# Kernel tuning notes

Measured on AMD Instinct MI355X. Metric: run time of the kernel, lower is better.

Reference implementation:

```python
import math
import jax, jax.numpy as jnp
import numpy as np

B, I, D, H, K, MAXI, FF = 2, 1024, 1024, 16, 64, 1024, 4096
DH = D // H
EPS = 1e-5

def _ln(x, g, b):
    m = x.mean(-1, keepdims=True)
    v = ((x - m) ** 2).mean(-1, keepdims=True)
    return (x - m) / jnp.sqrt(v + EPS) * g + b

def setup_inputs() -> dict:
    key = jax.random.key(0)
    ks = jax.random.split(key, 16)
    p = lambda i, sh: (0.02 * jax.random.normal(ks[i], sh)).astype(jnp.float32)
    # clamped relative-position indices: clamp(j - floor(1.0*i), -K, K) + K
    ar = np.arange(MAXI)
    idx = np.clip(ar[None, :] - ar[:, None], -K, K) + K  # [maxI, maxI]
    return {
        'x': jax.random.normal(ks[0], (B, I, D), dtype=jnp.float32),
        'j': jax.random.normal(ks[1], (B, I, D), dtype=jnp.float32),
        'ln1_g': jnp.ones((D,), jnp.float32), 'ln1_b': jnp.zeros((D,), jnp.float32),
        'Wv_w': p(2, (D, D)), 'Wv_b': jnp.zeros((D,), jnp.float32),
        'Wg_w': p(3, (D, D)), 'Wg_b': jnp.zeros((D,), jnp.float32),
        'lnv_g': jnp.ones((D,), jnp.float32), 'lnv_b': jnp.zeros((D,), jnp.float32),
        'Wq1_w': p(4, (D, D)), 'Wq1_b': jnp.zeros((D,), jnp.float32),
        'Wk_w': p(5, (D, D)), 'Wk_b': jnp.zeros((D,), jnp.float32),
        'Wq2_w': p(6, (D, D)), 'Wq2_b': jnp.zeros((D,), jnp.float32),
        'rel_emb': p(7, (2 * K + 1, D)),
        'Wo_w': p(8, (D, D)), 'Wo_b': jnp.zeros((D,), jnp.float32),
        'ln2_g': jnp.ones((D,), jnp.float32), 'ln2_b': jnp.zeros((D,), jnp.float32),
        'ff1_w': p(9, (D, FF)), 'ff1_b': jnp.zeros((FF,), jnp.float32),
        'ff2_w': p(10, (FF, D)), 'ff2_b': jnp.zeros((D,), jnp.float32),
        'indices': jnp.asarray(idx, jnp.int32),
    }

def reference(x, j, ln1_g, ln1_b, Wv_w, Wv_b, Wg_w, Wg_b, lnv_g, lnv_b,
              Wq1_w, Wq1_b, Wk_w, Wk_b, Wq2_w, Wq2_b, rel_emb,
              Wo_w, Wo_b, ln2_g, ln2_b, ff1_w, ff1_b, ff2_w, ff2_b, indices):
    Bv, Iq, _ = x.shape
    res = x
    xn = _ln(x, ln1_g, ln1_b)
    # value / gate streams with gelu activation, layernorm on v only
    v = _ln(jax.nn.gelu(xn @ Wv_w + Wv_b, approximate=False), lnv_g, lnv_b)
    g = jax.nn.gelu(xn @ Wg_w + Wg_b, approximate=False)
    vh = v.reshape(Bv, -1, H, DH)   # [B,J,H,Dh]
    gh = g.reshape(Bv, -1, H, DH)   # [B,I,H,Dh]
    # absolute-position scores: Q1(j) . K(j)^T
    q1 = (j @ Wq1_w + Wq1_b).reshape(Bv, -1, H, DH)
    kh = (j @ Wk_w + Wk_b).reshape(Bv, -1, H, DH)
    aa = jnp.einsum('bihd,bjhd->bhij', q1, kh)  # [B,H,I,J]
    # relative-position scores: Q2(j) . rel_embed^T, gathered by clamped indices
    q2 = (j @ Wq2_w + Wq2_b).reshape(Bv, -1, H, DH)
    rh = rel_emb.reshape(2 * K + 1, H, DH)
    arf = jnp.einsum('bihd,rhd->bhir', q2, rh)  # [B,H,I,2K+1]
    Jk = kh.shape[1]
    idx = jnp.broadcast_to(indices[None, None, :Iq, :Jk], (Bv, H, Iq, Jk))
    ar = jnp.take_along_axis(arf, idx, axis=-1)  # [B,H,I,J]
    a = jax.nn.softmax((aa + ar) / math.sqrt(DH), axis=-1)
    o = jnp.einsum('bhij,bjhd->bihd', a, vh) * gh  # gated attention output
    o = o.reshape(Bv, -1, D) @ Wo_w + Wo_b
    x1 = o + res
    # feed-forward sublayer
    h = jax.nn.relu(_ln(x1, ln2_g, ln2_b) @ ff1_w + ff1_b)
    out = h @ ff2_w + ff2_b + x1
    return (out, a)
```

## Files before the change

kernel.cpp:

```cpp
#include <hip/hip_runtime.h>
#include <hip/hip_bf16.h>
#include <math.h>

#define D_   1024
#define H_   16
#define DH_  64
#define FF_  4096
#define R_   129
#define I_   1024
#define B_   2
#define MROWS 2048
#define QKVLD 3072

typedef __bf16 v8bf16 __attribute__((ext_vector_type(8)));
typedef float f32x4 __attribute__((ext_vector_type(4)));

__device__ __forceinline__ float gelu_f(float x) {
    return 0.5f * x * (1.0f + erff(x * 0.7071067811865476f));
}

__device__ __forceinline__ void ldsld16(const void* g, void* l) {
    __builtin_amdgcn_global_load_lds(
        (const __attribute__((address_space(1))) void*)g,
        (__attribute__((address_space(3))) void*)l, 16, 0, 0);
}

__global__ __launch_bounds__(256) void cvt_bf16(const float* __restrict__ in,
        __hip_bfloat16* __restrict__ out, int n4) {
    int i = blockIdx.x * 256 + threadIdx.x;
    if (i >= n4) return;
    float4 v = reinterpret_cast<const float4*>(in)[i];
    union { __hip_bfloat16 h[4]; uint2 u; } pk;
    pk.h[0] = __float2bfloat16(v.x); pk.h[1] = __float2bfloat16(v.y);
    pk.h[2] = __float2bfloat16(v.z); pk.h[3] = __float2bfloat16(v.w);
    reinterpret_cast<uint2*>(out)[i] = pk.u;
}

__global__ __launch_bounds__(256) void cvt_rel_bias(const float* __restrict__ rel,
        __hip_bfloat16* __restrict__ relb,
        const float* __restrict__ q1b_, const float* __restrict__ kb_,
        const float* __restrict__ q2b_, const float* __restrict__ vb_,
        const float* __restrict__ gb_,
        float* __restrict__ bias3, float* __restrict__ bias2) {
    int bid = blockIdx.x, t = threadIdx.x;
    if (bid < 129) {
        int i = bid * 256 + t;
        float4 v = reinterpret_cast<const float4*>(rel)[i];
        union { __hip_bfloat16 h[4]; uint2 u; } pk;
        pk.h[0] = __float2bfloat16(v.x); pk.h[1] = __float2bfloat16(v.y);
        pk.h[2] = __float2bfloat16(v.z); pk.h[3] = __float2bfloat16(v.w);
        reinterpret_cast<uint2*>(relb)[i] = pk.u;
    } else {
        int k = bid - 129;
        const float* src = k == 0 ? q1b_ : k == 1 ? kb_ : k == 2 ? q2b_ : k == 3 ? vb_ : gb_;
        float* dst = (k < 3 ? bias3 + k * D_ : bias2 + (k - 3) * D_);
        reinterpret_cast<float4*>(dst)[t] = reinterpret_cast<const float4*>(src)[t];
    }
}

__global__ __launch_bounds__(256) void wtrans6(
        const float* __restrict__ s0, const float* __restrict__ s1,
        const float* __restrict__ s2, const float* __restrict__ s3,
        const float* __restrict__ s4, const float* __restrict__ s5,
        __hip_bfloat16* __restrict__ d0, __hip_bfloat16* __restrict__ d1,
        __hip_bfloat16* __restrict__ d2, __hip_bfloat16* __restrict__ d3,
        __hip_bfloat16* __restrict__ d4, __hip_bfloat16* __restrict__ d5) {
    __shared__ float T[64][65];
    int z = blockIdx.z;
    const float* W = z == 0 ? s0 : z == 1 ? s1 : z == 2 ? s2 : z == 3 ? s3 : z == 4 ? s4 : s5;
    __hip_bfloat16* WT = z == 0 ? d0 : z == 1 ? d1 : z == 2 ? d2 : z == 3 ? d3 : z == 4 ? d4 : d5;
    int k0 = blockIdx.y * 64, n0 = blockIdx.x * 64;
    int t = threadIdx.x;
#pragma unroll
    for (int i = 0; i < 16; i++) {
        int e = t + i * 256, r = e >> 6, c = e & 63;
        T[r][c] = W[(size_t)(k0 + r) * D_ + n0 + c];
    }
    __syncthreads();
#pragma unroll
    for (int i = 0; i < 16; i++) {
        int e = t + i * 256, r = e >> 6, c = e & 63;
        WT[(size_t)(n0 + r) * D_ + k0 + c] = __float2bfloat16(T[c][r]);
    }
}

__global__ __launch_bounds__(256) void wtrans_ff(
        const float* __restrict__ f1, const float* __restrict__ f2,
        __hip_bfloat16* __restrict__ d1, __hip_bfloat16* __restrict__ d2) {
    __shared__ float T[64][65];
    int z = blockIdx.z;
    const float* W = z == 0 ? f1 : f2;
    __hip_bfloat16* WT = z == 0 ? d1 : d2;
    int K = z == 0 ? D_ : FF_;
    int N = z == 0 ? FF_ : D_;
    int k0 = (z == 0 ? blockIdx.y : blockIdx.x) * 64;
    int n0 = (z == 0 ? blockIdx.x : blockIdx.y) * 64;
    int t = threadIdx.x;
#pragma unroll
    for (int i = 0; i < 16; i++) {
        int e = t + i * 256, r = e >> 6, c = e & 63;
        T[r][c] = W[(size_t)(k0 + r) * N + n0 + c];
    }
    __syncthreads();
#pragma unroll
    for (int i = 0; i < 16; i++) {
        int e = t + i * 256, r = e >> 6, c = e & 63;
        WT[(size_t)(n0 + r) * K + k0 + c] = __float2bfloat16(T[c][r]);
    }
}

__global__ __launch_bounds__(256) void vtrans(const float* __restrict__ v,
        __hip_bfloat16* __restrict__ vt) {
    __shared__ float T[64][65];
    int z = blockIdx.y, b = z >> 4, h = z & 15;
    int j0 = blockIdx.x * 64;
    int t = threadIdx.x;
#pragma unroll
    for (int i = 0; i < 16; i++) {
        int e = t + i * 256, r = e >> 6, c = e & 63;
        T[r][c] = v[(size_t)(b * I_ + j0 + r) * D_ + h * DH_ + c];
    }
    __syncthreads();
#pragma unroll
    for (int i = 0; i < 16; i++) {
        int e = t + i * 256, r = e >> 6, c = e & 63;
        vt[((size_t)z * DH_ + r) * I_ + j0 + c] = __float2bfloat16(T[c][r]);
    }
}

template<int MR, int NWC, int ACT, int RES, int OUTBF>
__global__ __launch_bounds__(256) void gemm_mfma(
        const __hip_bfloat16* __restrict__ A,
        const __hip_bfloat16* __restrict__ Bt,
        const float* __restrict__ bias,
        const float* __restrict__ res,
        void* __restrict__ Cout,
        int N, int Kd, int lda, int ldb, int ldc,
        size_t sAb, size_t sAh, size_t sBb, size_t sBh, size_t sCz) {
    constexpr int NWR = 4 / NWC;
    constexpr int BM = NWR * MR * 16;
    constexpr int BN = NWC * 64;
    __shared__ __align__(16) __hip_bfloat16 As[BM * 64];
    __shared__ __align__(16) __hip_bfloat16 Bs[BN * 64];
    const char* AsB = (const char*)As;
    const char* BsB = (const char*)Bs;
    int z = blockIdx.z;
    const __hip_bfloat16* Ab = A + (size_t)(z >> 4) * sAb + (size_t)(z & 15) * sAh;
    const __hip_bfloat16* Bb = Bt + (size_t)(z >> 4) * sBb + (size_t)(z & 15) * sBh;
    float* Cf = (float*)Cout + (size_t)z * sCz;
    __hip_bfloat16* Cb = (__hip_bfloat16*)Cout + (size_t)z * sCz;
    int m0 = blockIdx.y * BM, n0 = blockIdx.x * BN;
    int t = threadIdx.x;
    int l = t & 63, w = t >> 6;
    int wr = w / NWC, wc = w % NWC;
    int lr = l & 15, kq = l >> 4;
    int rx = lr & 7;

    f32x4 acc[MR][4] = {};

    for (int k0 = 0; k0 < Kd; k0 += 64) {
#pragma unroll
        for (int i = 0; i < BM / 32; i++) {
            int e = t + i * 256;
            int row = e >> 3, sl = e & 7;
            int kb = sl ^ (row & 7);
            ldsld16(Ab + (size_t)(m0 + row) * lda + (k0 + kb * 8), (void*)(AsB + e * 16));
        }
#pragma unroll
        for (int i = 0; i < BN / 32; i++) {
            int e = t + i * 256;
            int row = e >> 3, sl = e & 7;
            int kb = sl ^ (row & 7);
            int nr = n0 + row; if (nr > N - 1) nr = N - 1;
            ldsld16(Bb + (size_t)nr * ldb + (k0 + kb * 8), (void*)(BsB + e * 16));
        }
        __syncthreads();
#pragma unroll
        for (int kc = 0; kc < 2; kc++) {
            int sloff = (((kc << 2) + kq) ^ rx) << 4;
            v8bf16 af[MR], bfr[4];
#pragma unroll
            for (int mr = 0; mr < MR; mr++)
                af[mr] = *(const v8bf16*)(AsB + ((wr * (MR * 16) + mr * 16 + lr) << 7) + sloff);
#pragma unroll
            for (int nc = 0; nc < 4; nc++)
                bfr[nc] = *(const v8bf16*)(BsB + ((wc * 64 + nc * 16 + lr) << 7) + sloff);
#pragma unroll
            for (int mr = 0; mr < MR; mr++)
#pragma unroll
                for (int nc = 0; nc < 4; nc++)
                    acc[mr][nc] = __builtin_amdgcn_mfma_f32_16x16x32_bf16(
                        af[mr], bfr[nc], acc[mr][nc], 0, 0, 0);
        }
        __syncthreads();
    }

#pragma unroll
    for (int mr = 0; mr < MR; mr++) {
        int rbase = m0 + wr * (MR * 16) + mr * 16 + kq * 4;
#pragma unroll
        for (int nc = 0; nc < 4; nc++) {
            int col = n0 + wc * 64 + nc * 16 + lr;
            bool okc = col < N;
            float bv = (bias && okc) ? bias[col] : 0.f;
#pragma unroll
            for (int ri = 0; ri < 4; ri++) {
                int r = rbase + ri;
                float val = acc[mr][nc][ri] + bv;
                if (ACT == 1) val = gelu_f(val);
                if (ACT == 2) val = fmaxf(val, 0.f);
                if (RES) val += res[(size_t)r * ldc + col];
                if (okc) {
                    if (OUTBF == 2) {
                        if (col < D_) Cf[(size_t)r * ldc + col] = val;
                        else ((__hip_bfloat16*)res)[(size_t)r * ldc + (col - D_)] =
                                 __float2bfloat16(val);
                    } else if (OUTBF == 1) {
                        Cb[(size_t)r * ldc + col] = __float2bfloat16(val);
                    } else {
                        Cf[(size_t)r * ldc + col] = val;
                    }
                }
            }
        }
    }
}

#define FA_AR 0
#define FA_K  16896
#define FA_V  (16896 + 8192)
#define FA_P  (16896 + 16384)
#define SC2   0.1803368801111244f
__global__ __launch_bounds__(256) void flash_attn3(
        const __hip_bfloat16* __restrict__ qkv,
        const __hip_bfloat16* __restrict__ vt,
        const __hip_bfloat16* __restrict__ arfb,
        const __hip_bfloat16* __restrict__ gb,
        float* __restrict__ a_out,
        __hip_bfloat16* __restrict__ obuf) {
    __shared__ __align__(16) char lds[16896 + 8192 * 3];
    __hip_bfloat16* arl = (__hip_bfloat16*)(lds + FA_AR);
    char* kB = lds + FA_K;
    char* vB = lds + FA_V;
    char* pB = lds + FA_P;

    int z = blockIdx.y, b = z >> 4, h = z & 15;
    int i0 = blockIdx.x * 64;
    int t = threadIdx.x, l = t & 63, w = t >> 6;
    int lr = l & 15, kq = l >> 4;

#pragma unroll
    for (int i = 0; i < 2; i++) {
        int e = t + i * 256;
        int row = e >> 3, sl = e & 7;
        int kb = sl ^ (row & 7);
        ldsld16(qkv + (size_t)(b * I_ + i0 + row) * QKVLD + h * DH_ + kb * 8,
                (void*)(pB + e * 16));
    }
    for (int idx = t; idx < 64 * 132; idx += 256) {
        int row = idx / 132, r = idx - row * 132;
        if (r < R_) arl[idx] = arfb[((size_t)z * I_ + i0 + row) * R_ + r];
    }
    __syncthreads();
    v8bf16 qf[2];
#pragma unroll
    for (int kc = 0; kc < 2; kc++)
        qf[kc] = *(const v8bf16*)(pB + ((w * 16 + lr) << 7) + ((((kc << 2) + kq) ^ (lr & 7)) << 4));

    int irow = w * 16 + kq * 4;
    int ig = i0 + irow;
    float loS[4], hiS[4];
#pragma unroll
    for (int ri = 0; ri < 4; ri++) {
        loS[ri] = __bfloat162float(arl[(irow + ri) * 132 + 0])   * SC2;
        hiS[ri] = __bfloat162float(arl[(irow + ri) * 132 + 128]) * SC2;
    }

    float l_ln[4] = {0.f, 0.f, 0.f, 0.f};
    for (int jt = 0; jt < 16; jt++) {
        int j0 = jt * 64;
#pragma unroll
        for (int i = 0; i < 2; i++) {
            int e = t + i * 256;
            int row = e >> 3, sl = e & 7;
            int kb = sl ^ (row & 7);
            ldsld16(qkv + (size_t)(b * I_ + j0 + row) * QKVLD + D_ + h * DH_ + kb * 8,
                    (void*)(kB + e * 16));
        }
        __syncthreads();
        f32x4 acc[4] = {};
        __builtin_amdgcn_s_setprio(1);
#pragma unroll
        for (int kc = 0; kc < 2; kc++) {
            int sloff = ((((kc << 2) + kq)) ^ (lr & 7)) << 4;
#pragma unroll
            for (int tt = 0; tt < 4; tt++) {
                v8bf16 kf = *(const v8bf16*)(kB + ((tt * 16 + lr) << 7) + sloff);
                acc[tt] = __builtin_amdgcn_mfma_f32_16x16x32_bf16(qf[kc], kf, acc[tt], 0, 0, 0);
            }
        }
        __builtin_amdgcn_s_setprio(0);
#pragma unroll
        for (int ri = 0; ri < 4; ri++) {
            int i_g = ig + ri;
            float sc[4];
            bool lo_all = (j0 + 63) <= (i_g - 64);
            bool hi_all = j0 >= (i_g + 64);
            if (lo_all || hi_all) {
                float c = lo_all ? loS[ri] : hiS[ri];
#pragma unroll
                for (int tt = 0; tt < 4; tt++) sc[tt] = fmaf(acc[tt][ri], SC2, c);
            } else {
#pragma unroll
                for (int tt = 0; tt < 4; tt++) {
                    int rel = j0 + tt * 16 + lr - i_g;
                    rel = rel < -64 ? -64 : (rel > 64 ? 64 : rel);
                    sc[tt] = (acc[tt][ri] + __bfloat162float(arl[(irow + ri) * 132 + rel + 64])) * SC2;
                }
            }
            l_ln[ri] += exp2f(sc[0]) + exp2f(sc[1]) + exp2f(sc[2]) + exp2f(sc[3]);
        }
        __syncthreads();
    }
    float offb[4];
#pragma unroll
    for (int ri = 0; ri < 4; ri++) {
        float s = l_ln[ri];
#pragma unroll
        for (int off = 1; off < 16; off <<= 1) s += __shfl_xor(s, off, 64);
        offb[ri] = __log2f(s);
    }

    f32x4 oacc[4] = {};
    for (int jt = 0; jt < 16; jt++) {
        int j0 = jt * 64;
#pragma unroll
        for (int i = 0; i < 2; i++) {
            int e = t + i * 256;
            int row = e >> 3, sl = e & 7;
            int kb = sl ^ (row & 7);
            ldsld16(qkv + (size_t)(b * I_ + j0 + row) * QKVLD + D_ + h * DH_ + kb * 8,
                    (void*)(kB + e * 16));
            ldsld16(vt + ((size_t)z * DH_ + row) * I_ + j0 + kb * 8,
                    (void*)(vB + e * 16));
        }
        __syncthreads();
        f32x4 acc[4] = {};
        __builtin_amdgcn_s_setprio(1);
#pragma unroll
        for (int kc = 0; kc < 2; kc++) {
            int sloff = ((((kc << 2) + kq)) ^ (lr & 7)) << 4;
#pragma unroll
            for (int tt = 0; tt < 4; tt++) {
                v8bf16 kf = *(const v8bf16*)(kB + ((tt * 16 + lr) << 7) + sloff);
                acc[tt] = __builtin_amdgcn_mfma_f32_16x16x32_bf16(qf[kc], kf, acc[tt], 0, 0, 0);
            }
        }
        __builtin_amdgcn_s_setprio(0);
#pragma unroll
        for (int ri = 0; ri < 4; ri++) {
            int i_g = ig + ri;
            int rowl = irow + ri;
            float sc[4];
            bool lo_all = (j0 + 63) <= (i_g - 64);
            bool hi_all = j0 >= (i_g + 64);
            if (lo_all || hi_all) {
                float c = lo_all ? loS[ri] : hiS[ri];
#pragma unroll
                for (int tt = 0; tt < 4; tt++) sc[tt] = fmaf(acc[tt][ri], SC2, c);
            } else {
#pragma unroll
                for (int tt = 0; tt < 4; tt++) {
                    int rel = j0 + tt * 16 + lr - i_g;
                    rel = rel < -64 ? -64 : (rel > 64 ? 64 : rel);
                    sc[tt] = (acc[tt][ri] + __bfloat162float(arl[rowl * 132 + rel + 64])) * SC2;
                }
            }
            float* gout = a_out + ((size_t)z * I_ + i0 + rowl) * I_ + j0;
#pragma unroll
            for (int tt = 0; tt < 4; tt++) {
                float p = exp2f(sc[tt] - offb[ri]);
                __builtin_nontemporal_store(p, gout + tt * 16 + lr);
                *(__hip_bfloat16*)(pB + (rowl << 7) +
                        ((((tt * 2) + (lr >> 3)) ^ (rowl & 7)) << 4) + (lr & 7) * 2) =
                    __float2bfloat16(p);
            }
        }
        __syncthreads();
        __builtin_amdgcn_s_setprio(1);
#pragma unroll
        for (int kc = 0; kc < 2; kc++) {
            int sloff = ((((kc << 2) + kq)) ^ (lr & 7)) << 4;
            v8bf16 pf = *(const v8bf16*)(pB + ((w * 16 + lr) << 7) + sloff);
#pragma unroll
            for (int nc = 0; nc < 4; nc++) {
                v8bf16 vf = *(const v8bf16*)(vB + ((nc * 16 + lr) << 7) + sloff);
                oacc[nc] = __builtin_amdgcn_mfma_f32_16x16x32_bf16(pf, vf, oacc[nc], 0, 0, 0);
            }
        }
        __builtin_amdgcn_s_setprio(0);
        __syncthreads();
    }
#pragma unroll
    for (int nc = 0; nc < 4; nc++) {
#pragma unroll
        for (int ri = 0; ri < 4; ri++) {
            int r = i0 + irow + ri;
            size_t oi = ((size_t)(b * I_ + r)) * D_ + h * DH_ + nc * 16 + lr;
            obuf[oi] = __float2bfloat16(oacc[nc][ri] * __bfloat162float(gb[oi]));
        }
    }
}

template<int OUTBF>
__global__ __launch_bounds__(256) void ln_kernel(const float* __restrict__ in,
        void* __restrict__ out, const float* __restrict__ gw,
        const float* __restrict__ bw) {
    __shared__ float shs[4], shq[4];
    int row = blockIdx.x;
    int t = threadIdx.x;
    float4 v = reinterpret_cast<const float4*>(in + (size_t)row * D_)[t];
    float s = v.x + v.y + v.z + v.w;
#pragma unroll
    for (int off = 32; off > 0; off >>= 1) s += __shfl_down(s, off, 64);
    if ((t & 63) == 0) shs[t >> 6] = s;
    __syncthreads();
    float mean = (shs[0] + shs[1] + shs[2] + shs[3]) * (1.0f / D_);
    float d0 = v.x - mean, d1 = v.y - mean, d2 = v.z - mean, d3 = v.w - mean;
    float q = d0 * d0 + d1 * d1 + d2 * d2 + d3 * d3;
#pragma unroll
    for (int off = 32; off > 0; off >>= 1) q += __shfl_down(q, off, 64);
    if ((t & 63) == 0) shq[t >> 6] = q;
    __syncthreads();
    float var = (shq[0] + shq[1] + shq[2] + shq[3]) * (1.0f / D_);
    float rstd = rsqrtf(var + 1e-5f);
    float4 g4 = reinterpret_cast<const float4*>(gw)[t];
    float4 b4 = reinterpret_cast<const float4*>(bw)[t];
    float o0 = d0 * rstd * g4.x + b4.x;
    float o1 = d1 * rstd * g4.y + b4.y;
    float o2 = d2 * rstd * g4.z + b4.z;
    float o3 = d3 * rstd * g4.w + b4.w;
    if (OUTBF) {
        union { __hip_bfloat16 h[4]; uint2 u; } pk;
        pk.h[0] = __float2bfloat16(o0); pk.h[1] = __float2bfloat16(o1);
        pk.h[2] = __float2bfloat16(o2); pk.h[3] = __float2bfloat16(o3);
        reinterpret_cast<uint2*>((__hip_bfloat16*)out + (size_t)row * D_)[t] = pk.u;
    } else {
        float4 o; o.x = o0; o.y = o1; o.z = o2; o.w = o3;
        reinterpret_cast<float4*>((float*)out + (size_t)row * D_)[t] = o;
    }
}

extern "C" void kernel_launch(void* const* d_in, const int* in_sizes, int n_in,
                              void* d_out, int out_size, void* d_ws, size_t ws_size,
                              hipStream_t stream) {
    const float* x      = (const float*)d_in[0];
    const float* jin    = (const float*)d_in[1];
    const float* ln1_g  = (const float*)d_in[2];
    const float* ln1_b  = (const float*)d_in[3];
    const float* Wv_w   = (const float*)d_in[4];
    const float* Wv_b   = (const float*)d_in[5];
    const float* Wg_w   = (const float*)d_in[6];
    const float* Wg_b   = (const float*)d_in[7];
    const float* lnv_g  = (const float*)d_in[8];
    const float* lnv_b  = (const float*)d_in[9];
    const float* Wq1_w  = (const float*)d_in[10];
    const float* Wq1_b  = (const float*)d_in[11];
    const float* Wk_w   = (const float*)d_in[12];
    const float* Wk_b   = (const float*)d_in[13];
    const float* Wq2_w  = (const float*)d_in[14];
    const float* Wq2_b  = (const float*)d_in[15];
    const float* rel    = (const float*)d_in[16];
    const float* Wo_w   = (const float*)d_in[17];
    const float* Wo_b   = (const float*)d_in[18];
    const float* ln2_g  = (const float*)d_in[19];
    const float* ln2_b  = (const float*)d_in[20];
    const float* ff1_w  = (const float*)d_in[21];
    const float* ff1_b  = (const float*)d_in[22];
    const float* ff2_w  = (const float*)d_in[23];
    const float* ff2_b  = (const float*)d_in[24];

    float* out0  = (float*)d_out;
    float* a_out = out0 + (size_t)B_ * I_ * D_;

    char* wsb = (char*)d_ws;
    const size_t MB = 1u << 20;
    __hip_bfloat16* wvwgT= (__hip_bfloat16*)(wsb + 0 * MB);
    __hip_bfloat16* qkvT = (__hip_bfloat16*)(wsb + 4 * MB);
    __hip_bfloat16* WoT  = (__hip_bfloat16*)(wsb + 10 * MB);
    __hip_bfloat16* ff1T = (__hip_bfloat16*)(wsb + 12 * MB);
    __hip_bfloat16* ff2T = (__hip_bfloat16*)(wsb + 20 * MB);
    __hip_bfloat16* jbf  = (__hip_bfloat16*)(wsb + 28 * MB);
    __hip_bfloat16* qkv  = (__hip_bfloat16*)(wsb + 32 * MB);
    __hip_bfloat16* relb = (__hip_bfloat16*)(wsb + 44 * MB);
    __hip_bfloat16* arfb = (__hip_bfloat16*)(wsb + 45 * MB);
    __hip_bfloat16* gbuf = (__hip_bfloat16*)(wsb + 54 * MB);
    float*          vbuf = (float*)        (wsb + 58 * MB);
    __hip_bfloat16* xnb  = (__hip_bfloat16*)(wsb + 28 * MB);
    __hip_bfloat16* vt   = (__hip_bfloat16*)(wsb + 28 * MB);
    __hip_bfloat16* obuf = (__hip_bfloat16*)(wsb + 58 * MB);
    float*          x1   = (float*)        (wsb + 32 * MB);
    __hip_bfloat16* x1nb = (__hip_bfloat16*)(wsb + 40 * MB);
    __hip_bfloat16* hbuf = (__hip_bfloat16*)(wsb + 44 * MB);
    float*          bias3= (float*)        (wsb + 66 * MB);
    float*          bias2= (float*)        (wsb + 66 * MB + 16384);

    dim3 blk(256);

    cvt_bf16<<<2048, blk, 0, stream>>>(jin, jbf, (MROWS * D_) / 4);
    cvt_rel_bias<<<134, blk, 0, stream>>>(rel, relb,
        Wq1_b, Wk_b, Wq2_b, Wv_b, Wg_b, bias3, bias2);
    wtrans6<<<dim3(16, 16, 6), blk, 0, stream>>>(
        Wq1_w, Wk_w, Wq2_w, Wv_w, Wg_w, Wo_w,
        qkvT, qkvT + 1024*1024, qkvT + 2048*1024,
        wvwgT, wvwgT + 1024*1024, WoT);
    wtrans_ff<<<dim3(64, 16, 2), blk, 0, stream>>>(ff1_w, ff2_w, ff1T, ff2T);

    gemm_mfma<4, 2, 0, 0, 1><<<dim3(24, 16, 1), blk, 0, stream>>>(
        jbf, qkvT, bias3, nullptr, qkv, QKVLD, D_, D_, D_, QKVLD, 0, 0, 0, 0, 0);
    gemm_mfma<4, 2, 0, 0, 1><<<dim3(2, 8, 32), blk, 0, stream>>>(
        qkv + 2 * D_, relb, nullptr, nullptr, arfb,
        R_, DH_, QKVLD, D_, R_,
        (size_t)I_ * QKVLD, (size_t)DH_, 0, (size_t)DH_, (size_t)I_ * R_);

    ln_kernel<1><<<MROWS, blk, 0, stream>>>(x, xnb, ln1_g, ln1_b);
    gemm_mfma<4, 2, 1, 0, 2><<<dim3(16, 16, 1), blk, 0, stream>>>(
        xnb, wvwgT, bias2, (const float*)gbuf, vbuf, 2 * D_, D_, D_, D_, D_, 0, 0, 0, 0, 0);
    ln_kernel<0><<<MROWS, blk, 0, stream>>>(vbuf, vbuf, lnv_g, lnv_b);
    vtrans<<<dim3(16, 32), blk, 0, stream>>>(vbuf, vt);

    flash_attn3<<<dim3(16, 32), blk, 0, stream>>>(qkv, vt, arfb, gbuf, a_out, obuf);

    gemm_mfma<2, 1, 0, 1, 0><<<dim3(16, 16, 1), blk, 0, stream>>>(
        obuf, WoT, Wo_b, x, x1, D_, D_, D_, D_, D_, 0, 0, 0, 0, 0);
    ln_kernel<1><<<MROWS, blk, 0, stream>>>(x1, x1nb, ln2_g, ln2_b);
    gemm_mfma<4, 2, 2, 0, 1><<<dim3(32, 16, 1), blk, 0, stream>>>(
        x1nb, ff1T, ff1_b, nullptr, hbuf, FF_, D_, D_, D_, FF_, 0, 0, 0, 0, 0);
    gemm_mfma<2, 1, 0, 1, 0><<<dim3(16, 16, 1), blk, 0, stream>>>(
        hbuf, ff2T, ff2_b, x1, out0, D_, FF_, FF_, FF_, D_, 0, 0, 0, 0, 0);
}
```

Before: 288.3 us.

## Double-buffer K and V tiles in flash attention to overlap loads with compute

The attention kernel now keeps two LDS buffers each for K and V tiles. It issues the async global-to-LDS load for the next tile while the current tile is being multiplied, in both the row-sum pass and the output pass. This hides global load latency and drops one barrier per iteration in each pass. In exchange, LDS use per block grows from about 41 KB to 57 KB, which can limit how many blocks share a CU, and correctness now depends on the barrier placement relative to the buffer swaps.

```diff
diff --git a/kernel.cpp b/kernel.cpp
--- a/kernel.cpp
+++ b/kernel.cpp
@@ -226,37 +226,49 @@
     }
 }
 
-#define FA_AR 0
-#define FA_K  16896
-#define FA_V  (16896 + 8192)
-#define FA_P  (16896 + 16384)
+#define FB_K0 16896
+#define FB_V0 33280
+#define FB_P  49664
 #define SC2   0.1803368801111244f
-__global__ __launch_bounds__(256) void flash_attn3(
+__global__ __launch_bounds__(256) void flash_attn4(
         const __hip_bfloat16* __restrict__ qkv,
         const __hip_bfloat16* __restrict__ vt,
         const __hip_bfloat16* __restrict__ arfb,
         const __hip_bfloat16* __restrict__ gb,
         float* __restrict__ a_out,
         __hip_bfloat16* __restrict__ obuf) {
-    __shared__ __align__(16) char lds[16896 + 8192 * 3];
-    __hip_bfloat16* arl = (__hip_bfloat16*)(lds + FA_AR);
-    char* kB = lds + FA_K;
-    char* vB = lds + FA_V;
-    char* pB = lds + FA_P;
+    __shared__ __align__(16) char lds[57856];
+    __hip_bfloat16* arl = (__hip_bfloat16*)lds;
+    char* pB = lds + FB_P;
 
     int z = blockIdx.y, b = z >> 4, h = z & 15;
     int i0 = blockIdx.x * 64;
     int t = threadIdx.x, l = t & 63, w = t >> 6;
     int lr = l & 15, kq = l >> 4;
+    const __hip_bfloat16* Kg = qkv + (size_t)(b * I_) * QKVLD + D_ + h * DH_;
+    const __hip_bfloat16* Vg = vt + (size_t)z * DH_ * I_;
+
+#define STG_K(j0v, off) { \
+    _Pragma("unroll") for (int i_ = 0; i_ < 2; i_++) { \
+        int e_ = t + i_ * 256, row_ = e_ >> 3, sl_ = e_ & 7; \
+        int kb_ = sl_ ^ (row_ & 7); \
+        ldsld16(Kg + (size_t)((j0v) + row_) * QKVLD + kb_ * 8, \
+                (void*)(lds + (off) + e_ * 16)); } }
+#define STG_V(j0v, off) { \
+    _Pragma("unroll") for (int i_ = 0; i_ < 2; i_++) { \
+        int e_ = t + i_ * 256, row_ = e_ >> 3, sl_ = e_ & 7; \
+        int kb_ = sl_ ^ (row_ & 7); \
+        ldsld16(Vg + (size_t)row_ * I_ + (j0v) + kb_ * 8, \
+                (void*)(lds + (off) + e_ * 16)); } }
 
 #pragma unroll
     for (int i = 0; i < 2; i++) {
-        int e = t + i * 256;
-        int row = e >> 3, sl = e & 7;
+        int e = t + i * 256, row = e >> 3, sl = e & 7;
         int kb = sl ^ (row & 7);
         ldsld16(qkv + (size_t)(b * I_ + i0 + row) * QKVLD + h * DH_ + kb * 8,
                 (void*)(pB + e * 16));
     }
+    STG_K(0, FB_K0);
     for (int idx = t; idx < 64 * 132; idx += 256) {
         int row = idx / 132, r = idx - row * 132;
         if (r < R_) arl[idx] = arfb[((size_t)z * I_ + i0 + row) * R_ + r];
@@ -277,17 +289,11 @@
     }
 
     float l_ln[4] = {0.f, 0.f, 0.f, 0.f};
+    int cur = 0;
     for (int jt = 0; jt < 16; jt++) {
+        if (jt < 15) STG_K((jt + 1) * 64, FB_K0 + ((cur ^ 1) << 13));
+        const char* kB = lds + FB_K0 + (cur << 13);
         int j0 = jt * 64;
-#pragma unroll
-        for (int i = 0; i < 2; i++) {
-            int e = t + i * 256;
-            int row = e >> 3, sl = e & 7;
-            int kb = sl ^ (row & 7);
-            ldsld16(qkv + (size_t)(b * I_ + j0 + row) * QKVLD + D_ + h * DH_ + kb * 8,
-                    (void*)(kB + e * 16));
-        }
-        __syncthreads();
         f32x4 acc[4] = {};
         __builtin_amdgcn_s_setprio(1);
 #pragma unroll
@@ -321,7 +327,10 @@
             l_ln[ri] += exp2f(sc[0]) + exp2f(sc[1]) + exp2f(sc[2]) + exp2f(sc[3]);
         }
         __syncthreads();
-    }
+        cur ^= 1;
+    }
+    STG_K(0, FB_K0);
+    STG_V(0, FB_V0);
     float offb[4];
 #pragma unroll
     for (int ri = 0; ri < 4; ri++) {
@@ -330,21 +339,15 @@
         for (int off = 1; off < 16; off <<= 1) s += __shfl_xor(s, off, 64);
         offb[ri] = __log2f(s);
     }
+    __syncthreads();
 
     f32x4 oacc[4] = {};
+    int kcur = 0, vcur = 0;
     for (int jt = 0; jt < 16; jt++) {
+        if (jt < 15) STG_K((jt + 1) * 64, FB_K0 + ((kcur ^ 1) << 13));
+        const char* kB = lds + FB_K0 + (kcur << 13);
+        const char* vB = lds + FB_V0 + (vcur << 13);
         int j0 = jt * 64;
-#pragma unroll
-        for (int i = 0; i < 2; i++) {
-            int e = t + i * 256;
-            int row = e >> 3, sl = e & 7;
-            int kb = sl ^ (row & 7);
-            ldsld16(qkv + (size_t)(b * I_ + j0 + row) * QKVLD + D_ + h * DH_ + kb * 8,
-                    (void*)(kB + e * 16));
-            ldsld16(vt + ((size_t)z * DH_ + row) * I_ + j0 + kb * 8,
-                    (void*)(vB + e * 16));
-        }
-        __syncthreads();
         f32x4 acc[4] = {};
         __builtin_amdgcn_s_setprio(1);
 #pragma unroll
@@ -387,6 +390,7 @@
             }
         }
         __syncthreads();
+        if (jt < 15) STG_V((jt + 1) * 64, FB_V0 + ((vcur ^ 1) << 13));
         __builtin_amdgcn_s_setprio(1);
 #pragma unroll
         for (int kc = 0; kc < 2; kc++) {
@@ -399,7 +403,7 @@
             }
         }
         __builtin_amdgcn_s_setprio(0);
-        __syncthreads();
+        kcur ^= 1; vcur ^= 1;
     }
 #pragma unroll
     for (int nc = 0; nc < 4; nc++) {
@@ -410,6 +414,8 @@
             obuf[oi] = __float2bfloat16(oacc[nc][ri] * __bfloat162float(gb[oi]));
         }
     }
+#undef STG_K
+#undef STG_V
 }
 
 template<int OUTBF>
@@ -529,7 +535,7 @@
     ln_kernel<0><<<MROWS, blk, 0, stream>>>(vbuf, vbuf, lnv_g, lnv_b);
     vtrans<<<dim3(16, 32), blk, 0, stream>>>(vbuf, vt);
 
-    flash_attn3<<<dim3(16, 32), blk, 0, stream>>>(qkv, vt, arfb, gbuf, a_out, obuf);
+    flash_attn4<<<dim3(16, 32), blk, 0, stream>>>(qkv, vt, arfb, gbuf, a_out, obuf);
 
     gemm_mfma<2, 1, 0, 1, 0><<<dim3(16, 16, 1), blk, 0, stream>>>(
         obuf, WoT, Wo_b, x, x1, D_, D_, D_, D_, D_, 0, 0, 0, 0, 0);
```

Measured after the change: 289.9 us. Within noise of the previous version (+0.6%).

## Enlarge attention query tile to 128 rows with 512-thread blocks sharing K/V tiles

Applied to the files above, without the earlier changes.

The flash attention kernel now processes 128 query rows per block with 8 waves instead of 64 rows with 4 waves. Each K and V tile loaded into LDS is therefore reused by twice as many query rows, halving global K/V traffic. The relative-position table is also stored more compactly, holding only the 127 interior offsets, with the clamped edge values taken from registers. In exchange the grid shrinks to 256 blocks and each block uses close to 64KB of LDS, which lowers occupancy and may leave CUs underfilled.

```diff
diff --git a/kernel.cpp b/kernel.cpp
--- a/kernel.cpp
+++ b/kernel.cpp
@@ -226,40 +226,42 @@
     }
 }
 
-#define FA_AR 0
-#define FA_K  16896
-#define FA_V  (16896 + 8192)
-#define FA_P  (16896 + 16384)
+#define F5_K  32512
+#define F5_V  40704
+#define F5_P  48896
 #define SC2   0.1803368801111244f
-__global__ __launch_bounds__(256) void flash_attn3(
+__global__ __launch_bounds__(512) void flash_attn5(
         const __hip_bfloat16* __restrict__ qkv,
         const __hip_bfloat16* __restrict__ vt,
         const __hip_bfloat16* __restrict__ arfb,
         const __hip_bfloat16* __restrict__ gb,
         float* __restrict__ a_out,
         __hip_bfloat16* __restrict__ obuf) {
-    __shared__ __align__(16) char lds[16896 + 8192 * 3];
-    __hip_bfloat16* arl = (__hip_bfloat16*)(lds + FA_AR);
-    char* kB = lds + FA_K;
-    char* vB = lds + FA_V;
-    char* pB = lds + FA_P;
+    __shared__ __align__(16) char lds[65280];
+    __hip_bfloat16* arl = (__hip_bfloat16*)lds;
+    char* kB = lds + F5_K;
+    char* vB = lds + F5_V;
+    char* pB = lds + F5_P;
 
     int z = blockIdx.y, b = z >> 4, h = z & 15;
-    int i0 = blockIdx.x * 64;
+    int i0 = blockIdx.x * 128;
     int t = threadIdx.x, l = t & 63, w = t >> 6;
     int lr = l & 15, kq = l >> 4;
+    const __hip_bfloat16* Kg = qkv + (size_t)(b * I_) * QKVLD + D_ + h * DH_;
+    const __hip_bfloat16* Vg = vt + (size_t)z * DH_ * I_;
+    const __hip_bfloat16* arz = arfb + (size_t)z * I_ * R_;
 
 #pragma unroll
     for (int i = 0; i < 2; i++) {
-        int e = t + i * 256;
+        int e = t + i * 512;
         int row = e >> 3, sl = e & 7;
         int kb = sl ^ (row & 7);
         ldsld16(qkv + (size_t)(b * I_ + i0 + row) * QKVLD + h * DH_ + kb * 8,
                 (void*)(pB + e * 16));
     }
-    for (int idx = t; idx < 64 * 132; idx += 256) {
-        int row = idx / 132, r = idx - row * 132;
-        if (r < R_) arl[idx] = arfb[((size_t)z * I_ + i0 + row) * R_ + r];
+    for (int idx = t; idx < 128 * 127; idx += 512) {
+        int row = idx / 127, rm = idx - row * 127;
+        arl[idx] = arz[((size_t)(i0 + row)) * R_ + rm + 1];
     }
     __syncthreads();
     v8bf16 qf[2];
@@ -272,20 +274,17 @@
     float loS[4], hiS[4];
 #pragma unroll
     for (int ri = 0; ri < 4; ri++) {
-        loS[ri] = __bfloat162float(arl[(irow + ri) * 132 + 0])   * SC2;
-        hiS[ri] = __bfloat162float(arl[(irow + ri) * 132 + 128]) * SC2;
+        loS[ri] = __bfloat162float(arz[((size_t)(ig + ri)) * R_ + 0])   * SC2;
+        hiS[ri] = __bfloat162float(arz[((size_t)(ig + ri)) * R_ + 128]) * SC2;
     }
 
     float l_ln[4] = {0.f, 0.f, 0.f, 0.f};
     for (int jt = 0; jt < 16; jt++) {
         int j0 = jt * 64;
-#pragma unroll
-        for (int i = 0; i < 2; i++) {
-            int e = t + i * 256;
-            int row = e >> 3, sl = e & 7;
+        {
+            int row = t >> 3, sl = t & 7;
             int kb = sl ^ (row & 7);
-            ldsld16(qkv + (size_t)(b * I_ + j0 + row) * QKVLD + D_ + h * DH_ + kb * 8,
-                    (void*)(kB + e * 16));
+            ldsld16(Kg + (size_t)(j0 + row) * QKVLD + kb * 8, (void*)(kB + t * 16));
         }
         __syncthreads();
         f32x4 acc[4] = {};
@@ -313,9 +312,10 @@
             } else {
 #pragma unroll
                 for (int tt = 0; tt < 4; tt++) {
-                    int rel = j0 + tt * 16 + lr - i_g;
-                    rel = rel < -64 ? -64 : (rel > 64 ? 64 : rel);
-                    sc[tt] = (acc[tt][ri] + __bfloat162float(arl[(irow + ri) * 132 + rel + 64])) * SC2;
+                    int reln = j0 + tt * 16 + lr - i_g;
+                    float arv = reln <= -64 ? loS[ri] : (reln >= 64 ? hiS[ri] :
+                        __bfloat162float(arl[(irow + ri) * 127 + reln + 63]) * SC2);
+                    sc[tt] = fmaf(acc[tt][ri], SC2, arv);
                 }
             }
             l_ln[ri] += exp2f(sc[0]) + exp2f(sc[1]) + exp2f(sc[2]) + exp2f(sc[3]);
@@ -334,15 +334,11 @@
     f32x4 oacc[4] = {};
     for (int jt = 0; jt < 16; jt++) {
         int j0 = jt * 64;
-#pragma unroll
-        for (int i = 0; i < 2; i++) {
-            int e = t + i * 256;
-            int row = e >> 3, sl = e & 7;
+        {
+            int row = t >> 3, sl = t & 7;
             int kb = sl ^ (row & 7);
-            ldsld16(qkv + (size_t)(b * I_ + j0 + row) * QKVLD + D_ + h * DH_ + kb * 8,
-                    (void*)(kB + e * 16));
-            ldsld16(vt + ((size_t)z * DH_ + row) * I_ + j0 + kb * 8,
-                    (void*)(vB + e * 16));
+            ldsld16(Kg + (size_t)(j0 + row) * QKVLD + kb * 8, (void*)(kB + t * 16));
+            ldsld16(Vg + (size_t)row * I_ + j0 + kb * 8, (void*)(vB + t * 16));
         }
         __syncthreads();
         f32x4 acc[4] = {};
@@ -371,9 +367,10 @@
             } else {
 #pragma unroll
                 for (int tt = 0; tt < 4; tt++) {
-                    int rel = j0 + tt * 16 + lr - i_g;
-                    rel = rel < -64 ? -64 : (rel > 64 ? 64 : rel);
-                    sc[tt] = (acc[tt][ri] + __bfloat162float(arl[rowl * 132 + rel + 64])) * SC2;
+                    int reln = j0 + tt * 16 + lr - i_g;
+                    float arv = reln <= -64 ? loS[ri] : (reln >= 64 ? hiS[ri] :
+                        __bfloat162float(arl[rowl * 127 + reln + 63]) * SC2);
+                    sc[tt] = fmaf(acc[tt][ri], SC2, arv);
                 }
             }
             float* gout = a_out + ((size_t)z * I_ + i0 + rowl) * I_ + j0;
@@ -529,7 +526,7 @@
     ln_kernel<0><<<MROWS, blk, 0, stream>>>(vbuf, vbuf, lnv_g, lnv_b);
     vtrans<<<dim3(16, 32), blk, 0, stream>>>(vbuf, vt);
 
-    flash_attn3<<<dim3(16, 32), blk, 0, stream>>>(qkv, vt, arfb, gbuf, a_out, obuf);
+    flash_attn5<<<dim3(8, 32), dim3(512), 0, stream>>>(qkv, vt, arfb, gbuf, a_out, obuf);
 
     gemm_mfma<2, 1, 0, 1, 0><<<dim3(16, 16, 1), blk, 0, stream>>>(
         obuf, WoT, Wo_b, x, x1, D_, D_, D_, D_, D_, 0, 0, 0, 0, 0);
```

Result: slower. 296.0 us (+2.7%).
